# Kernel optimization log

Hardware: AMD Instinct MI355X
Metric: run time of the kernel (lower is better)

The kernel has to match this reference:

```python
import jax, jax.numpy as jnp
import numpy as np

N_NODES = 10000
N_EDGES = 640000
D = 128


def _sage_conv(x, src, dst, W_l, b, W_r):
    # PyG SAGEConv (mean aggr): out = lin_l(mean_{j in N(i)} x_j) + lin_r(x_i)
    msgs = x[src]                                        # [E, D_in] gather
    agg = jax.ops.segment_sum(msgs, dst, num_segments=N_NODES)  # [N, D_in]
    deg = jax.ops.segment_sum(jnp.ones((src.shape[0],), x.dtype), dst,
                              num_segments=N_NODES)
    agg = agg / jnp.maximum(deg, 1.0)[:, None]           # mean; isolated nodes -> 0
    return agg @ W_l + b + x @ W_r


def setup_inputs() -> dict:
    key = jax.random.key(0)
    ks = jax.random.split(key, 8)
    s = 1.0 / np.sqrt(D)
    return {
        "x": jax.random.normal(ks[0], (N_NODES, D), dtype=jnp.float32),
        "edge_index": jax.random.randint(ks[1], (2, N_EDGES), 0, N_NODES, dtype=jnp.int64),
        "W_l0": jax.random.normal(ks[2], (D, D), dtype=jnp.float32) * s,
        "b0": jnp.zeros((D,), dtype=jnp.float32),
        "W_r0": jax.random.normal(ks[3], (D, D), dtype=jnp.float32) * s,
        "W_l1": jax.random.normal(ks[4], (D, D), dtype=jnp.float32) * s,
        "b1": jnp.zeros((D,), dtype=jnp.float32),
        "W_r1": jax.random.normal(ks[5], (D, D), dtype=jnp.float32) * s,
    }


def reference(x, edge_index, W_l0, b0, W_r0, W_l1, b1, W_r1):
    # Dropout(p=0.3) is identity in eval mode (reference runs inference math).
    src, dst = edge_index[0], edge_index[1]
    h = jax.nn.elu(_sage_conv(x, src, dst, W_l0, b0, W_r0))
    h = jax.nn.elu(_sage_conv(h, src, dst, W_l1, b1, W_r1))
    return h
```

## Files before the change

### kernel.cpp

```cpp
#include <hip/hip_runtime.h>

#define N_NODES 10000
#define N_EDGES 640000
#define D 128
#define MAXDEG 128
#define NBUCK 157
#define BCAP 6144
#define EPT 5
#define ZROW 10000

typedef unsigned int uint;
typedef unsigned short u16;
typedef short bf16x8 __attribute__((ext_vector_type(8)));
typedef float f32x4 __attribute__((ext_vector_type(4)));

__device__ __forceinline__ u16 f2bf(float f) {
    uint u = __float_as_uint(f);
    return (u16)((u + 0x7fffu + ((u >> 16) & 1u)) >> 16);
}
__device__ __forceinline__ float bflo(uint v) { return __uint_as_float(v << 16); }
__device__ __forceinline__ float bfhi(uint v) { return __uint_as_float(v & 0xffff0000u); }

__device__ __forceinline__ int edge_at(const void* ei, int is32, int idx) {
    if (is32) return ((const int*)ei)[idx];
    return (int)((const long long*)ei)[idx];
}

__global__ __launch_bounds__(256)
void binp1_kernel(const void* __restrict__ ei, int* __restrict__ gcount,
                  uint* __restrict__ gbucket) {
    __shared__ int hist[NBUCK];
    __shared__ int base[NBUCK];
    __shared__ int s_is32;
    const int t = threadIdx.x;
    if (t < NBUCK) hist[t] = 0;
    if (t == 0) s_is32 = 0;
    __syncthreads();
    const int e0 = blockIdx.x * (256 * EPT);
    if (((const int*)ei)[2 * (e0 + t) + 1] != 0) s_is32 = 1;
    __syncthreads();
    const int is32 = s_is32;
    uint pk[EPT];
    int  rk[EPT];
#pragma unroll
    for (int i = 0; i < EPT; ++i) {
        int e  = e0 + i * 256 + t;
        int s  = edge_at(ei, is32, e);
        int dn = edge_at(ei, is32, N_EDGES + e);
        pk[i] = ((uint)dn << 16) | (uint)s;
        rk[i] = atomicAdd(&hist[dn >> 6], 1);
    }
    __syncthreads();
    if (t < NBUCK) base[t] = atomicAdd(&gcount[t], hist[t]);
    __syncthreads();
#pragma unroll
    for (int i = 0; i < EPT; ++i) {
        int bkt = (int)(pk[i] >> 22);
        int pos = base[bkt] + rk[i];
        if (pos < BCAP) gbucket[(size_t)bkt * BCAP + pos] = pk[i];
    }
}

__global__ __launch_bounds__(256)
void prep_kernel(const int* __restrict__ gcount, const uint* __restrict__ gbucket,
                 u16* __restrict__ adj, int* __restrict__ deg_g,
                 const float* __restrict__ x, uint* __restrict__ xb2,
                 const float* __restrict__ Wl0, const float* __restrict__ Wr0,
                 const float* __restrict__ Wl1, const float* __restrict__ Wr1,
                 u16* __restrict__ WT0, u16* __restrict__ WT1) {
    const int b = blockIdx.x;
    const int t = threadIdx.x;
    __shared__ __align__(16) u16 tile[64][MAXDEG];
    __shared__ int cur[64];
    if (b < NBUCK) {
        uint* tw = (uint*)&tile[0][0];
#pragma unroll
        for (int q = 0; q < 16; ++q) tw[t + q * 256] = ((uint)ZROW << 16) | ZROW;
        if (t < 64) cur[t] = 0;
        __syncthreads();
        const int total = min(gcount[b], BCAP);
        for (int e = t; e < total; e += 256) {
            uint pk = gbucket[(size_t)b * BCAP + e];
            int ln = (int)((pk >> 16) & 63u);
            int r = atomicAdd(&cur[ln], 1);
            if (r < MAXDEG) tile[ln][r] = (u16)(pk & 0xffffu);
        }
        __syncthreads();
        const int node0 = b * 64;
        if (t < 64 && node0 + t < N_NODES) deg_g[node0 + t] = cur[t];
        const uint4* ts = (const uint4*)&tile[0][0];
#pragma unroll
        for (int q = 0; q < 4; ++q) {
            int i = t + q * 256;
            int node = node0 + (i >> 4);
            if (node < N_NODES) ((uint4*)(adj + (size_t)node * MAXDEG))[i & 15] = ts[i];
        }
    } else if (b < NBUCK + 625) {
        int idx = (b - NBUCK) * 256 + t;
        const float4* p = (const float4*)x + (size_t)idx * 2;
        float4 a = p[0], bb = p[1];
        uint4 r;
        r.x = (uint)f2bf(a.x) | ((uint)f2bf(a.y) << 16);
        r.y = (uint)f2bf(a.z) | ((uint)f2bf(a.w) << 16);
        r.z = (uint)f2bf(bb.x) | ((uint)f2bf(bb.y) << 16);
        r.w = (uint)f2bf(bb.z) | ((uint)f2bf(bb.w) << 16);
        ((uint4*)xb2)[idx] = r;
    } else if (b < NBUCK + 625 + 256) {
        int b2 = b - (NBUCK + 625);
        int layer = b2 >> 7, d = b2 & 127, k = t;
        const float* Wl = layer ? Wl1 : Wl0;
        const float* Wr = layer ? Wr1 : Wr0;
        u16* WT = layer ? WT1 : WT0;
        float v = (k < 128) ? Wl[k * D + d] : Wr[(k - 128) * D + d];
        WT[(size_t)d * 256 + k] = f2bf(v);
    } else {
        if (t < 16) ((uint4*)(xb2 + (size_t)ZROW * 64))[t] = make_uint4(0, 0, 0, 0);
    }
}

__global__ __launch_bounds__(256)
void fused_layer_kernel(const uint* __restrict__ src2, const u16* __restrict__ adj,
                        const int* __restrict__ deg_g, const u16* __restrict__ WT,
                        const float* __restrict__ bias,
                        float* __restrict__ outf ,
                        u16* __restrict__ outb ) {
    __shared__ __align__(16) u16 A_lds[4][256];
    const int t = threadIdx.x;
    const int w = t >> 6, l = t & 63;
    const int nb = blockIdx.x * 4;
    const int node = nb + w;

    const int g = l >> 4, c = l & 15;
    const int half = g >> 1, sh = (g & 1) << 4;
    const int dg = deg_g[node];
    const int cnt = min(dg, MAXDEG);
    const uint4* __restrict__ rowq = (const uint4*)(adj + (size_t)node * MAXDEG);
    float acc[8];
#pragma unroll
    for (int i = 0; i < 8; ++i) acc[i] = 0.f;
    const int nch = (cnt + 15) >> 4;
#pragma unroll 2
    for (int ch = 0; ch < nch; ++ch) {
        uint4 wa = rowq[2 * ch];
        uint4 wb = rowq[2 * ch + 1];
        uint a0 = half ? wa.y : wa.x;
        uint a1 = half ? wa.w : wa.z;
        uint b0 = half ? wb.y : wb.x;
        uint b1 = half ? wb.w : wb.z;
        uint id0 = (a0 >> sh) & 0xffffu;
        uint id1 = (a1 >> sh) & 0xffffu;
        uint id2 = (b0 >> sh) & 0xffffu;
        uint id3 = (b1 >> sh) & 0xffffu;
        uint4 v0 = ((const uint4*)(src2 + (size_t)id0 * 64))[c];
        uint4 v1 = ((const uint4*)(src2 + (size_t)id1 * 64))[c];
        uint4 v2 = ((const uint4*)(src2 + (size_t)id2 * 64))[c];
        uint4 v3 = ((const uint4*)(src2 + (size_t)id3 * 64))[c];
        acc[0] += bflo(v0.x) + bflo(v1.x) + bflo(v2.x) + bflo(v3.x);
        acc[1] += bfhi(v0.x) + bfhi(v1.x) + bfhi(v2.x) + bfhi(v3.x);
        acc[2] += bflo(v0.y) + bflo(v1.y) + bflo(v2.y) + bflo(v3.y);
        acc[3] += bfhi(v0.y) + bfhi(v1.y) + bfhi(v2.y) + bfhi(v3.y);
        acc[4] += bflo(v0.z) + bflo(v1.z) + bflo(v2.z) + bflo(v3.z);
        acc[5] += bfhi(v0.z) + bfhi(v1.z) + bfhi(v2.z) + bfhi(v3.z);
        acc[6] += bflo(v0.w) + bflo(v1.w) + bflo(v2.w) + bflo(v3.w);
        acc[7] += bfhi(v0.w) + bfhi(v1.w) + bfhi(v2.w) + bfhi(v3.w);
    }
#pragma unroll
    for (int i = 0; i < 8; ++i) {
        float r = acc[i];
        r += __shfl_xor(r, 16, 64);
        r += __shfl_xor(r, 32, 64);
        acc[i] = r;
    }
    char* arow = (char*)&A_lds[w][0];
    const int swz = w << 4;
    if (g == 0) {
        float inv = 1.0f / fmaxf((float)dg, 1.0f);
        uint4 o;
        o.x = (uint)f2bf(acc[0] * inv) | ((uint)f2bf(acc[1] * inv) << 16);
        o.y = (uint)f2bf(acc[2] * inv) | ((uint)f2bf(acc[3] * inv) << 16);
        o.z = (uint)f2bf(acc[4] * inv) | ((uint)f2bf(acc[5] * inv) << 16);
        o.w = (uint)f2bf(acc[6] * inv) | ((uint)f2bf(acc[7] * inv) << 16);
        *(uint4*)(arow + ((c * 16) ^ swz)) = o;
    }
    if (l < 16) {
        uint4 vx = ((const uint4*)(src2 + (size_t)node * 64))[l];
        *(uint4*)(arow + ((256 + l * 16) ^ swz)) = vx;
    }
    __syncthreads();

    const int lr = l & 15, q = l >> 4;
    f32x4 acc0 = {0.f, 0.f, 0.f, 0.f}, acc1 = {0.f, 0.f, 0.f, 0.f};
    const u16* wt0 = WT + (size_t)(w * 32 + lr) * 256;
    const u16* wt1 = WT + (size_t)(w * 32 + 16 + lr) * 256;
    const char* abase = (const char*)&A_lds[lr & 3][0];
    const int aswz = (lr & 3) << 4;
#pragma unroll
    for (int kk = 0; kk < 8; ++kk) {
        bf16x8 af = {0, 0, 0, 0, 0, 0, 0, 0};
        if (lr < 4) af = *(const bf16x8*)(abase + ((kk * 64 + q * 16) ^ aswz));
        bf16x8 bf0 = *(const bf16x8*)(wt0 + kk * 32 + q * 8);
        bf16x8 bf1 = *(const bf16x8*)(wt1 + kk * 32 + q * 8);
        acc0 = __builtin_amdgcn_mfma_f32_16x16x32_bf16(af, bf0, acc0, 0, 0, 0);
        acc1 = __builtin_amdgcn_mfma_f32_16x16x32_bf16(af, bf1, acc1, 0, 0, 0);
    }
    if (q == 0) {
        const int col0 = w * 32 + lr, col1 = col0 + 16;
        const float b0v = bias[col0], b1v = bias[col1];
#pragma unroll
        for (int j = 0; j < 4; ++j) {
            const int nd = nb + j;
            float v0 = acc0[j] + b0v; v0 = v0 > 0.f ? v0 : expm1f(v0);
            float v1 = acc1[j] + b1v; v1 = v1 > 0.f ? v1 : expm1f(v1);
            if (outf) {
                outf[(size_t)nd * D + col0] = v0;
                outf[(size_t)nd * D + col1] = v1;
            }
            if (outb) {
                outb[(size_t)nd * D + col0] = f2bf(v0);
                outb[(size_t)nd * D + col1] = f2bf(v1);
            }
        }
    }
    if (outb && blockIdx.x == 0 && t < 16)
        ((uint4*)(outb + (size_t)ZROW * D))[t] = make_uint4(0, 0, 0, 0);
}

extern "C" void kernel_launch(void* const* d_in, const int* in_sizes, int n_in,
                              void* d_out, int out_size, void* d_ws, size_t ws_size,
                              hipStream_t stream) {
    const float* x   = (const float*)d_in[0];
    const void*  ei  = d_in[1];
    const float* Wl0 = (const float*)d_in[2];
    const float* b0  = (const float*)d_in[3];
    const float* Wr0 = (const float*)d_in[4];
    const float* Wl1 = (const float*)d_in[5];
    const float* b1  = (const float*)d_in[6];
    const float* Wr1 = (const float*)d_in[7];
    float* out = (float*)d_out;

    char* ws = (char*)d_ws;
    int*  gcount  = (int*)(ws + 1024);
    int*  deg     = (int*)(ws + 4096);
    u16*  adj     = (u16*)(ws + 65536);
    uint* gbucket = (uint*)(ws + 3145728);
    uint* xb2     = (uint*)(ws + 7340032);
    uint* yb2     = (uint*)(ws + 10485760);
    u16*  WT0     = (u16*)(ws + 13631488);
    u16*  WT1     = (u16*)(ws + 13697024);

    hipMemsetAsync(ws, 0, 4096, stream);

    binp1_kernel<<<500, 256, 0, stream>>>(ei, gcount, gbucket);
    prep_kernel<<<NBUCK + 625 + 256 + 1, 256, 0, stream>>>(
        gcount, gbucket, adj, deg, x, xb2, Wl0, Wr0, Wl1, Wr1, WT0, WT1);

    fused_layer_kernel<<<2500, 256, 0, stream>>>(xb2, adj, deg, WT0, b0,
                                                 (float*)0, (u16*)yb2);
    fused_layer_kernel<<<2500, 256, 0, stream>>>(yb2, adj, deg, WT1, b1,
                                                 out, (u16*)0);
}
```

Before: 95.71 us.

## Merge all stages into one cooperative persistent kernel with grid syncs

Replaces the four kernel launches with a single cooperative mega-kernel that bins edges, converts x and the weights, sorts buckets, and runs both SAGE layers, separated by grid.sync barriers. It is meant to remove launch gaps and tail effects between stages. The fused layer now handles 16 nodes per tile, so the MFMA uses all 16 rows instead of 4 with zero padding. A fallback path using separate gather and GEMM kernels is kept. The grid-wide barriers and the limited number of resident persistent blocks (512) could reduce gather parallelism compared with 2500 blocks.

```diff
diff --git a/kernel.cpp b/kernel.cpp
--- a/kernel.cpp
+++ b/kernel.cpp
@@ -1,4 +1,7 @@
 #include <hip/hip_runtime.h>
+#include <hip/hip_cooperative_groups.h>
+
+namespace cg = cooperative_groups;
 
 #define N_NODES 10000
 #define N_EDGES 640000
@@ -6,8 +9,9 @@
 #define MAXDEG 128
 #define NBUCK 157
 #define BCAP 6144
-#define EPT 5
 #define ZROW 10000
+#define NCHUNK 500
+#define CH_E 1280
 
 typedef unsigned int uint;
 typedef unsigned short u16;
@@ -26,24 +30,18 @@
     return (int)((const long long*)ei)[idx];
 }
 
-__global__ __launch_bounds__(256)
-void binp1_kernel(const void* __restrict__ ei, int* __restrict__ gcount,
-                  uint* __restrict__ gbucket) {
-    __shared__ int hist[NBUCK];
-    __shared__ int base[NBUCK];
-    __shared__ int s_is32;
+
+__device__ __forceinline__ void bin_chunk(const void* __restrict__ ei, int is32,
+                                          int chunk, int* hist, int* base,
+                                          int* __restrict__ gcount,
+                                          uint* __restrict__ gbucket) {
     const int t = threadIdx.x;
     if (t < NBUCK) hist[t] = 0;
-    if (t == 0) s_is32 = 0;
-    __syncthreads();
-    const int e0 = blockIdx.x * (256 * EPT);
-    if (((const int*)ei)[2 * (e0 + t) + 1] != 0) s_is32 = 1;
-    __syncthreads();
-    const int is32 = s_is32;
-    uint pk[EPT];
-    int  rk[EPT];
-#pragma unroll
-    for (int i = 0; i < EPT; ++i) {
+    __syncthreads();
+    const int e0 = chunk * CH_E;
+    uint pk[5]; int rk[5];
+#pragma unroll
+    for (int i = 0; i < 5; ++i) {
         int e  = e0 + i * 256 + t;
         int s  = edge_at(ei, is32, e);
         int dn = edge_at(ei, is32, N_EDGES + e);
@@ -54,85 +52,49 @@
     if (t < NBUCK) base[t] = atomicAdd(&gcount[t], hist[t]);
     __syncthreads();
 #pragma unroll
-    for (int i = 0; i < EPT; ++i) {
+    for (int i = 0; i < 5; ++i) {
         int bkt = (int)(pk[i] >> 22);
         int pos = base[bkt] + rk[i];
         if (pos < BCAP) gbucket[(size_t)bkt * BCAP + pos] = pk[i];
     }
 }
 
-__global__ __launch_bounds__(256)
-void prep_kernel(const int* __restrict__ gcount, const uint* __restrict__ gbucket,
-                 u16* __restrict__ adj, int* __restrict__ deg_g,
-                 const float* __restrict__ x, uint* __restrict__ xb2,
-                 const float* __restrict__ Wl0, const float* __restrict__ Wr0,
-                 const float* __restrict__ Wl1, const float* __restrict__ Wr1,
-                 u16* __restrict__ WT0, u16* __restrict__ WT1) {
-    const int b = blockIdx.x;
-    const int t = threadIdx.x;
-    __shared__ __align__(16) u16 tile[64][MAXDEG];
-    __shared__ int cur[64];
-    if (b < NBUCK) {
-        uint* tw = (uint*)&tile[0][0];
-#pragma unroll
-        for (int q = 0; q < 16; ++q) tw[t + q * 256] = ((uint)ZROW << 16) | ZROW;
-        if (t < 64) cur[t] = 0;
-        __syncthreads();
-        const int total = min(gcount[b], BCAP);
-        for (int e = t; e < total; e += 256) {
-            uint pk = gbucket[(size_t)b * BCAP + e];
-            int ln = (int)((pk >> 16) & 63u);
-            int r = atomicAdd(&cur[ln], 1);
-            if (r < MAXDEG) tile[ln][r] = (u16)(pk & 0xffffu);
-        }
-        __syncthreads();
-        const int node0 = b * 64;
-        if (t < 64 && node0 + t < N_NODES) deg_g[node0 + t] = cur[t];
-        const uint4* ts = (const uint4*)&tile[0][0];
-#pragma unroll
-        for (int q = 0; q < 4; ++q) {
-            int i = t + q * 256;
-            int node = node0 + (i >> 4);
-            if (node < N_NODES) ((uint4*)(adj + (size_t)node * MAXDEG))[i & 15] = ts[i];
-        }
-    } else if (b < NBUCK + 625) {
-        int idx = (b - NBUCK) * 256 + t;
-        const float4* p = (const float4*)x + (size_t)idx * 2;
-        float4 a = p[0], bb = p[1];
-        uint4 r;
-        r.x = (uint)f2bf(a.x) | ((uint)f2bf(a.y) << 16);
-        r.y = (uint)f2bf(a.z) | ((uint)f2bf(a.w) << 16);
-        r.z = (uint)f2bf(bb.x) | ((uint)f2bf(bb.y) << 16);
-        r.w = (uint)f2bf(bb.z) | ((uint)f2bf(bb.w) << 16);
-        ((uint4*)xb2)[idx] = r;
-    } else if (b < NBUCK + 625 + 256) {
-        int b2 = b - (NBUCK + 625);
-        int layer = b2 >> 7, d = b2 & 127, k = t;
-        const float* Wl = layer ? Wl1 : Wl0;
-        const float* Wr = layer ? Wr1 : Wr0;
-        u16* WT = layer ? WT1 : WT0;
-        float v = (k < 128) ? Wl[k * D + d] : Wr[(k - 128) * D + d];
-        WT[(size_t)d * 256 + k] = f2bf(v);
-    } else {
-        if (t < 16) ((uint4*)(xb2 + (size_t)ZROW * 64))[t] = make_uint4(0, 0, 0, 0);
-    }
-}
-
-__global__ __launch_bounds__(256)
-void fused_layer_kernel(const uint* __restrict__ src2, const u16* __restrict__ adj,
-                        const int* __restrict__ deg_g, const u16* __restrict__ WT,
-                        const float* __restrict__ bias,
-                        float* __restrict__ outf ,
-                        u16* __restrict__ outb ) {
-    __shared__ __align__(16) u16 A_lds[4][256];
-    const int t = threadIdx.x;
-    const int w = t >> 6, l = t & 63;
-    const int nb = blockIdx.x * 4;
-    const int node = nb + w;
-
-    const int g = l >> 4, c = l & 15;
-    const int half = g >> 1, sh = (g & 1) << 4;
-    const int dg = deg_g[node];
+__device__ __forceinline__ void sort_bucket(char* smem, int b,
+                                            const int* __restrict__ gcount,
+                                            const uint* __restrict__ gbucket,
+                                            u16* __restrict__ adj,
+                                            int* __restrict__ deg_g) {
+    const int t = threadIdx.x;
+    u16 (*tile)[MAXDEG] = (u16 (*)[MAXDEG])smem;
+    int* cur = (int*)(smem + 16384);
+    uint* tw = (uint*)smem;
+#pragma unroll
+    for (int q = 0; q < 16; ++q) tw[t + q * 256] = ((uint)ZROW << 16) | ZROW;
+    if (t < 64) cur[t] = 0;
+    __syncthreads();
+    const int total = min(gcount[b], BCAP);
+    for (int e = t; e < total; e += 256) {
+        uint pk = gbucket[(size_t)b * BCAP + e];
+        int ln = (int)((pk >> 16) & 63u);
+        int r = atomicAdd(&cur[ln], 1);
+        if (r < MAXDEG) tile[ln][r] = (u16)(pk & 0xffffu);
+    }
+    __syncthreads();
+    const int node0 = b * 64;
+    if (t < 64 && node0 + t < N_NODES) deg_g[node0 + t] = cur[t];
+    const uint4* ts = (const uint4*)smem;
+#pragma unroll
+    for (int q = 0; q < 4; ++q) {
+        int i = t + q * 256;
+        int node = node0 + (i >> 4);
+        if (node < N_NODES) ((uint4*)(adj + (size_t)node * MAXDEG))[i & 15] = ts[i];
+    }
+}
+
+__device__ __forceinline__ void gather_node(const uint* __restrict__ src2,
+                                            const u16* __restrict__ adj,
+                                            int node, int dg, int g, int c,
+                                            int half, int sh, uint4* o) {
     const int cnt = min(dg, MAXDEG);
     const uint4* __restrict__ rowq = (const uint4*)(adj + (size_t)node * MAXDEG);
     float acc[8];
@@ -171,58 +133,232 @@
         r += __shfl_xor(r, 32, 64);
         acc[i] = r;
     }
-    char* arow = (char*)&A_lds[w][0];
-    const int swz = w << 4;
-    if (g == 0) {
-        float inv = 1.0f / fmaxf((float)dg, 1.0f);
-        uint4 o;
-        o.x = (uint)f2bf(acc[0] * inv) | ((uint)f2bf(acc[1] * inv) << 16);
-        o.y = (uint)f2bf(acc[2] * inv) | ((uint)f2bf(acc[3] * inv) << 16);
-        o.z = (uint)f2bf(acc[4] * inv) | ((uint)f2bf(acc[5] * inv) << 16);
-        o.w = (uint)f2bf(acc[6] * inv) | ((uint)f2bf(acc[7] * inv) << 16);
-        *(uint4*)(arow + ((c * 16) ^ swz)) = o;
-    }
-    if (l < 16) {
-        uint4 vx = ((const uint4*)(src2 + (size_t)node * 64))[l];
-        *(uint4*)(arow + ((256 + l * 16) ^ swz)) = vx;
-    }
-    __syncthreads();
-
+    float inv = 1.0f / fmaxf((float)dg, 1.0f);
+    o->x = (uint)f2bf(acc[0] * inv) | ((uint)f2bf(acc[1] * inv) << 16);
+    o->y = (uint)f2bf(acc[2] * inv) | ((uint)f2bf(acc[3] * inv) << 16);
+    o->z = (uint)f2bf(acc[4] * inv) | ((uint)f2bf(acc[5] * inv) << 16);
+    o->w = (uint)f2bf(acc[6] * inv) | ((uint)f2bf(acc[7] * inv) << 16);
+}
+
+__device__ __forceinline__ void gemm_tile(const u16* A, int nb,
+                                          const u16* __restrict__ WT,
+                                          const float* __restrict__ bias,
+                                          float* outf, u16* outb) {
+    const int t = threadIdx.x;
+    const int w = t >> 6, l = t & 63;
     const int lr = l & 15, q = l >> 4;
     f32x4 acc0 = {0.f, 0.f, 0.f, 0.f}, acc1 = {0.f, 0.f, 0.f, 0.f};
     const u16* wt0 = WT + (size_t)(w * 32 + lr) * 256;
     const u16* wt1 = WT + (size_t)(w * 32 + 16 + lr) * 256;
-    const char* abase = (const char*)&A_lds[lr & 3][0];
-    const int aswz = (lr & 3) << 4;
+    const char* abase = (const char*)(A + lr * 256);
+    const int aswz = (lr & 7) << 4;
 #pragma unroll
     for (int kk = 0; kk < 8; ++kk) {
-        bf16x8 af = {0, 0, 0, 0, 0, 0, 0, 0};
-        if (lr < 4) af = *(const bf16x8*)(abase + ((kk * 64 + q * 16) ^ aswz));
+        bf16x8 af  = *(const bf16x8*)(abase + ((kk * 64 + q * 16) ^ aswz));
         bf16x8 bf0 = *(const bf16x8*)(wt0 + kk * 32 + q * 8);
         bf16x8 bf1 = *(const bf16x8*)(wt1 + kk * 32 + q * 8);
         acc0 = __builtin_amdgcn_mfma_f32_16x16x32_bf16(af, bf0, acc0, 0, 0, 0);
         acc1 = __builtin_amdgcn_mfma_f32_16x16x32_bf16(af, bf1, acc1, 0, 0, 0);
     }
-    if (q == 0) {
-        const int col0 = w * 32 + lr, col1 = col0 + 16;
-        const float b0v = bias[col0], b1v = bias[col1];
-#pragma unroll
-        for (int j = 0; j < 4; ++j) {
-            const int nd = nb + j;
-            float v0 = acc0[j] + b0v; v0 = v0 > 0.f ? v0 : expm1f(v0);
-            float v1 = acc1[j] + b1v; v1 = v1 > 0.f ? v1 : expm1f(v1);
-            if (outf) {
-                outf[(size_t)nd * D + col0] = v0;
-                outf[(size_t)nd * D + col1] = v1;
-            }
-            if (outb) {
-                outb[(size_t)nd * D + col0] = f2bf(v0);
-                outb[(size_t)nd * D + col1] = f2bf(v1);
+    const int col0 = w * 32 + lr, col1 = col0 + 16;
+    const float b0v = bias[col0], b1v = bias[col1];
+#pragma unroll
+    for (int j = 0; j < 4; ++j) {
+        const int nd = nb + q * 4 + j;
+        float v0 = acc0[j] + b0v; v0 = v0 > 0.f ? v0 : expm1f(v0);
+        float v1 = acc1[j] + b1v; v1 = v1 > 0.f ? v1 : expm1f(v1);
+        if (outf) {
+            outf[(size_t)nd * D + col0] = v0;
+            outf[(size_t)nd * D + col1] = v1;
+        }
+        if (outb) {
+            outb[(size_t)nd * D + col0] = f2bf(v0);
+            outb[(size_t)nd * D + col1] = f2bf(v1);
+        }
+    }
+}
+
+__global__ __launch_bounds__(256)
+void binp1_kernel(const void* __restrict__ ei, int* __restrict__ gcount,
+                  uint* __restrict__ gbucket) {
+    __shared__ int hist[NBUCK];
+    __shared__ int base[NBUCK];
+    __shared__ int s_is32;
+    const int t = threadIdx.x;
+    if (t == 0) s_is32 = 0;
+    __syncthreads();
+    if (((const int*)ei)[2 * t + 1] != 0) s_is32 = 1;
+    __syncthreads();
+    bin_chunk(ei, s_is32, blockIdx.x, hist, base, gcount, gbucket);
+}
+
+__global__ __launch_bounds__(256)
+void prep_kernel(const int* __restrict__ gcount, const uint* __restrict__ gbucket,
+                 u16* __restrict__ adj, int* __restrict__ deg_g,
+                 const float* __restrict__ x, uint* __restrict__ xb2,
+                 const float* __restrict__ Wl0, const float* __restrict__ Wr0,
+                 const float* __restrict__ Wl1, const float* __restrict__ Wr1,
+                 u16* __restrict__ WT0, u16* __restrict__ WT1) {
+    __shared__ __align__(16) char smem[16640];
+    const int b = blockIdx.x;
+    const int t = threadIdx.x;
+    if (b < NBUCK) {
+        sort_bucket(smem, b, gcount, gbucket, adj, deg_g);
+    } else if (b < NBUCK + 625) {
+        int idx = (b - NBUCK) * 256 + t;
+        const float4* p = (const float4*)x + (size_t)idx * 2;
+        float4 a = p[0], bb = p[1];
+        uint4 r;
+        r.x = (uint)f2bf(a.x) | ((uint)f2bf(a.y) << 16);
+        r.y = (uint)f2bf(a.z) | ((uint)f2bf(a.w) << 16);
+        r.z = (uint)f2bf(bb.x) | ((uint)f2bf(bb.y) << 16);
+        r.w = (uint)f2bf(bb.z) | ((uint)f2bf(bb.w) << 16);
+        ((uint4*)xb2)[idx] = r;
+    } else if (b < NBUCK + 625 + 256) {
+        int b2 = b - (NBUCK + 625);
+        int layer = b2 >> 7, d = b2 & 127, k = t;
+        const float* Wl = layer ? Wl1 : Wl0;
+        const float* Wr = layer ? Wr1 : Wr0;
+        u16* WT = layer ? WT1 : WT0;
+        float v = (k < 128) ? Wl[k * D + d] : Wr[(k - 128) * D + d];
+        WT[(size_t)d * 256 + k] = f2bf(v);
+    } else {
+        if (t < 16) ((uint4*)(xb2 + (size_t)ZROW * 64))[t] = make_uint4(0, 0, 0, 0);
+    }
+}
+
+__global__ __launch_bounds__(256)
+void gather_kernel(const uint* __restrict__ xb2, const u16* __restrict__ adj,
+                   const int* __restrict__ deg_g, uint* __restrict__ aggb2) {
+    const int node = blockIdx.x * 4 + (threadIdx.x >> 6);
+    const int l = threadIdx.x & 63;
+    const int g = l >> 4, c = l & 15;
+    const int half = g >> 1, sh = (g & 1) << 4;
+    uint4 o;
+    gather_node(xb2, adj, node, deg_g[node], g, c, half, sh, &o);
+    if (g == 0) ((uint4*)(aggb2 + (size_t)node * 64))[c] = o;
+}
+
+__global__ __launch_bounds__(256)
+void mfma_gemm_kernel(const uint* __restrict__ aggb2, const uint* __restrict__ xb2,
+                      const u16* __restrict__ WT, const float* __restrict__ bias,
+                      float* __restrict__ outf, u16* __restrict__ outb) {
+    __shared__ __align__(16) u16 A_lds[16 * 256];
+    const int t = threadIdx.x;
+    const int nb = blockIdx.x * 16;
+    {
+        const int row = t >> 4, c = t & 15;
+        const int node = nb + row;
+        uint4 va = ((const uint4*)(aggb2 + (size_t)node * 64))[c];
+        uint4 vx = ((const uint4*)(xb2  + (size_t)node * 64))[c];
+        char* base = (char*)A_lds + row * 512;
+        const int swz = (row & 7) << 4;
+        *(uint4*)(base + ((c * 16) ^ swz))       = va;
+        *(uint4*)(base + ((256 + c * 16) ^ swz)) = vx;
+    }
+    __syncthreads();
+    gemm_tile(A_lds, nb, WT, bias, outf, outb);
+    if (outb && blockIdx.x == 0 && t < 16)
+        ((uint4*)(outb + (size_t)ZROW * D))[t] = make_uint4(0, 0, 0, 0);
+}
+
+__device__ __forceinline__ void fused_layer(char* smem, const uint* __restrict__ src2,
+                                            const u16* __restrict__ adj,
+                                            const int* __restrict__ deg_g,
+                                            const u16* __restrict__ WT,
+                                            const float* __restrict__ bias,
+                                            float* outf, u16* outb) {
+    const int t = threadIdx.x;
+    const int w = t >> 6, l = t & 63;
+    const int g = l >> 4, c = l & 15;
+    const int half = g >> 1, sh = (g & 1) << 4;
+    u16* A = (u16*)smem;
+
+    for (int tile = blockIdx.x; tile < 625; tile += gridDim.x) {
+        __syncthreads();
+        const int nb = tile * 16;
+        for (int i = 0; i < 4; ++i) {
+            const int li = w * 4 + i;
+            const int node = nb + li;
+            uint4 o;
+            gather_node(src2, adj, node, deg_g[node], g, c, half, sh, &o);
+            char* arow = (char*)(A + li * 256);
+            const int swz = (li & 7) << 4;
+            if (g == 0) *(uint4*)(arow + ((c * 16) ^ swz)) = o;
+            if (g == 1) {
+                uint4 vx = ((const uint4*)(src2 + (size_t)node * 64))[c];
+                *(uint4*)(arow + ((256 + c * 16) ^ swz)) = vx;
             }
         }
-    }
-    if (outb && blockIdx.x == 0 && t < 16)
-        ((uint4*)(outb + (size_t)ZROW * D))[t] = make_uint4(0, 0, 0, 0);
+        __syncthreads();
+        gemm_tile(A, nb, WT, bias, outf, outb);
+    }
+}
+
+__global__ __launch_bounds__(256, 2)
+void mega_kernel(const void* __restrict__ ei, int* __restrict__ gcount,
+                 uint* __restrict__ gbucket, u16* __restrict__ adj,
+                 int* __restrict__ deg_g, const float* __restrict__ x,
+                 uint* __restrict__ xb2, uint* __restrict__ yb2,
+                 const float* __restrict__ Wl0, const float* __restrict__ Wr0,
+                 const float* __restrict__ Wl1, const float* __restrict__ Wr1,
+                 u16* __restrict__ WT0, u16* __restrict__ WT1,
+                 const float* __restrict__ b0, const float* __restrict__ b1,
+                 float* __restrict__ out) {
+    __shared__ __align__(16) char smem[16640];
+    cg::grid_group grid = cg::this_grid();
+    const int t = threadIdx.x;
+    const int b = blockIdx.x;
+    const int nbk = gridDim.x;
+
+    {
+        int* hist = (int*)smem;
+        int* base = hist + NBUCK;
+        int* s32p = base + NBUCK;
+        if (t == 0) *s32p = 0;
+        __syncthreads();
+        if (((const int*)ei)[2 * t + 1] != 0) *s32p = 1;
+        __syncthreads();
+        const int is32 = *s32p;
+        for (int chunk = b; chunk < NCHUNK; chunk += nbk)
+            bin_chunk(ei, is32, chunk, hist, base, gcount, gbucket);
+    }
+    for (int idx = b * 256 + t; idx < N_NODES * D / 8; idx += nbk * 256) {
+        const float4* p = (const float4*)x + (size_t)idx * 2;
+        float4 a = p[0], bb = p[1];
+        uint4 r;
+        r.x = (uint)f2bf(a.x) | ((uint)f2bf(a.y) << 16);
+        r.y = (uint)f2bf(a.z) | ((uint)f2bf(a.w) << 16);
+        r.z = (uint)f2bf(bb.x) | ((uint)f2bf(bb.y) << 16);
+        r.w = (uint)f2bf(bb.z) | ((uint)f2bf(bb.w) << 16);
+        ((uint4*)xb2)[idx] = r;
+    }
+    for (int idx = b * 256 + t; idx < 2 * D * 256; idx += nbk * 256) {
+        int layer = idx >> 15;
+        int rem = idx & 32767;
+        int d = rem >> 8, k = rem & 255;
+        const float* Wl = layer ? Wl1 : Wl0;
+        const float* Wr = layer ? Wr1 : Wr0;
+        u16* WT = layer ? WT1 : WT0;
+        float v = (k < 128) ? Wl[k * D + d] : Wr[(k - 128) * D + d];
+        WT[(size_t)d * 256 + k] = f2bf(v);
+    }
+    if (b == 0 && t < 16) {
+        ((uint4*)(xb2 + (size_t)ZROW * 64))[t] = make_uint4(0, 0, 0, 0);
+        ((uint4*)(yb2 + (size_t)ZROW * 64))[t] = make_uint4(0, 0, 0, 0);
+    }
+    grid.sync();
+
+    for (int bk = b; bk < NBUCK; bk += nbk) {
+        __syncthreads();
+        sort_bucket(smem, bk, gcount, gbucket, adj, deg_g);
+    }
+    grid.sync();
+
+    fused_layer(smem, xb2, adj, deg_g, WT0, b0, (float*)0, (u16*)yb2);
+    grid.sync();
+
+    fused_layer(smem, yb2, adj, deg_g, WT1, b1, out, (u16*)0);
 }
 
 extern "C" void kernel_launch(void* const* d_in, const int* in_sizes, int n_in,
@@ -245,17 +381,37 @@
     uint* gbucket = (uint*)(ws + 3145728);
     uint* xb2     = (uint*)(ws + 7340032);
     uint* yb2     = (uint*)(ws + 10485760);
-    u16*  WT0     = (u16*)(ws + 13631488);
-    u16*  WT1     = (u16*)(ws + 13697024);
-
-    hipMemsetAsync(ws, 0, 4096, stream);
-
-    binp1_kernel<<<500, 256, 0, stream>>>(ei, gcount, gbucket);
-    prep_kernel<<<NBUCK + 625 + 256 + 1, 256, 0, stream>>>(
-        gcount, gbucket, adj, deg, x, xb2, Wl0, Wr0, Wl1, Wr1, WT0, WT1);
-
-    fused_layer_kernel<<<2500, 256, 0, stream>>>(xb2, adj, deg, WT0, b0,
-                                                 (float*)0, (u16*)yb2);
-    fused_layer_kernel<<<2500, 256, 0, stream>>>(yb2, adj, deg, WT1, b1,
-                                                 out, (u16*)0);
-}
+    uint* aggb2   = (uint*)(ws + 13631488);
+    u16*  WT0     = (u16*)(ws + 16777216);
+    u16*  WT1     = (u16*)(ws + 16842752);
+
+    (void)hipMemsetAsync(ws, 0, 4096, stream);
+
+    int maxB = 0;
+    if (hipOccupancyMaxActiveBlocksPerMultiprocessor(
+            &maxB, (const void*)mega_kernel, 256, 0) != hipSuccess)
+        maxB = 0;
+
+    hipError_t lerr = hipErrorUnknown;
+    if (maxB >= 1) {
+        int gridsz = (maxB >= 2) ? 512 : 256;
+        void* kargs[] = { (void*)&ei, (void*)&gcount, (void*)&gbucket, (void*)&adj,
+                          (void*)&deg, (void*)&x, (void*)&xb2, (void*)&yb2,
+                          (void*)&Wl0, (void*)&Wr0, (void*)&Wl1, (void*)&Wr1,
+                          (void*)&WT0, (void*)&WT1, (void*)&b0, (void*)&b1,
+                          (void*)&out };
+        lerr = hipLaunchCooperativeKernel((const void*)mega_kernel, dim3(gridsz),
+                                          dim3(256), kargs, 0, stream);
+    }
+    if (lerr != hipSuccess) {
+        binp1_kernel<<<NCHUNK, 256, 0, stream>>>(ei, gcount, gbucket);
+        prep_kernel<<<NBUCK + 625 + 256 + 1, 256, 0, stream>>>(
+            gcount, gbucket, adj, deg, x, xb2, Wl0, Wr0, Wl1, Wr1, WT0, WT1);
+        gather_kernel<<<2500, 256, 0, stream>>>(xb2, adj, deg, aggb2);
+        mfma_gemm_kernel<<<625, 256, 0, stream>>>(aggb2, xb2, WT0, b0,
+                                                  (float*)0, (u16*)yb2);
+        gather_kernel<<<2500, 256, 0, stream>>>(yb2, adj, deg, aggb2);
+        mfma_gemm_kernel<<<625, 256, 0, stream>>>(aggb2, yb2, WT1, b1,
+                                                  out, (u16*)0);
+    }
+}
```

Result: slower. 208.9 us (+118.2%).

## Process 16 nodes per block so MFMA tiles use all rows

Applied to the files above, without the earlier changes.

The fused layer kernel now uses 1024-thread blocks that aggregate 16 nodes, one per wave, into LDS. Eight waves then each run one 16x16x32 MFMA chain over all 16 rows, where before only 4 of 16 A rows were real nodes and the rest were zero padding. This removes wasted MFMA work and halves the weight loads per node. The zero-row write for the second layer's input moves into the prep kernel. The cost is a block-wide barrier over 16 waves with half of them idle during the matmul, and lower scheduling flexibility.

```diff
diff --git a/kernel.cpp b/kernel.cpp
--- a/kernel.cpp
+++ b/kernel.cpp
@@ -65,6 +65,7 @@
 void prep_kernel(const int* __restrict__ gcount, const uint* __restrict__ gbucket,
                  u16* __restrict__ adj, int* __restrict__ deg_g,
                  const float* __restrict__ x, uint* __restrict__ xb2,
+                 uint* __restrict__ yb2,
                  const float* __restrict__ Wl0, const float* __restrict__ Wr0,
                  const float* __restrict__ Wl1, const float* __restrict__ Wr1,
                  u16* __restrict__ WT0, u16* __restrict__ WT1) {
@@ -114,115 +115,107 @@
         float v = (k < 128) ? Wl[k * D + d] : Wr[(k - 128) * D + d];
         WT[(size_t)d * 256 + k] = f2bf(v);
     } else {
-        if (t < 16) ((uint4*)(xb2 + (size_t)ZROW * 64))[t] = make_uint4(0, 0, 0, 0);
-    }
-}
-
-__global__ __launch_bounds__(256)
-void fused_layer_kernel(const uint* __restrict__ src2, const u16* __restrict__ adj,
-                        const int* __restrict__ deg_g, const u16* __restrict__ WT,
-                        const float* __restrict__ bias,
-                        float* __restrict__ outf ,
-                        u16* __restrict__ outb ) {
-    __shared__ __align__(16) u16 A_lds[4][256];
+        if (t < 16) {
+            ((uint4*)(xb2 + (size_t)ZROW * 64))[t] = make_uint4(0, 0, 0, 0);
+            ((uint4*)(yb2 + (size_t)ZROW * 64))[t] = make_uint4(0, 0, 0, 0);
+        }
+    }
+}
+
+__global__ __launch_bounds__(1024, 8)
+void fused_kernel(const uint* __restrict__ src2, const u16* __restrict__ adj,
+                  const int* __restrict__ deg_g, const u16* __restrict__ WT,
+                  const float* __restrict__ bias,
+                  float* __restrict__ outf ,
+                  u16* __restrict__ outb ) {
+    __shared__ __align__(16) u16 A_lds[16 * 256];
     const int t = threadIdx.x;
     const int w = t >> 6, l = t & 63;
-    const int nb = blockIdx.x * 4;
+    const int nb = blockIdx.x * 16;
     const int node = nb + w;
 
-    const int g = l >> 4, c = l & 15;
-    const int half = g >> 1, sh = (g & 1) << 4;
-    const int dg = deg_g[node];
-    const int cnt = min(dg, MAXDEG);
-    const uint4* __restrict__ rowq = (const uint4*)(adj + (size_t)node * MAXDEG);
-    float acc[8];
-#pragma unroll
-    for (int i = 0; i < 8; ++i) acc[i] = 0.f;
-    const int nch = (cnt + 15) >> 4;
+    {
+        const int g = l >> 4, c = l & 15;
+        const int half = g >> 1, sh = (g & 1) << 4;
+        const int dg = deg_g[node];
+        const int cnt = min(dg, MAXDEG);
+        const uint4* __restrict__ rowq = (const uint4*)(adj + (size_t)node * MAXDEG);
+        float acc[8];
+#pragma unroll
+        for (int i = 0; i < 8; ++i) acc[i] = 0.f;
+        const int nch = (cnt + 15) >> 4;
 #pragma unroll 2
-    for (int ch = 0; ch < nch; ++ch) {
-        uint4 wa = rowq[2 * ch];
-        uint4 wb = rowq[2 * ch + 1];
-        uint a0 = half ? wa.y : wa.x;
-        uint a1 = half ? wa.w : wa.z;
-        uint b0 = half ? wb.y : wb.x;
-        uint b1 = half ? wb.w : wb.z;
-        uint id0 = (a0 >> sh) & 0xffffu;
-        uint id1 = (a1 >> sh) & 0xffffu;
-        uint id2 = (b0 >> sh) & 0xffffu;
-        uint id3 = (b1 >> sh) & 0xffffu;
-        uint4 v0 = ((const uint4*)(src2 + (size_t)id0 * 64))[c];
-        uint4 v1 = ((const uint4*)(src2 + (size_t)id1 * 64))[c];
-        uint4 v2 = ((const uint4*)(src2 + (size_t)id2 * 64))[c];
-        uint4 v3 = ((const uint4*)(src2 + (size_t)id3 * 64))[c];
-        acc[0] += bflo(v0.x) + bflo(v1.x) + bflo(v2.x) + bflo(v3.x);
-        acc[1] += bfhi(v0.x) + bfhi(v1.x) + bfhi(v2.x) + bfhi(v3.x);
-        acc[2] += bflo(v0.y) + bflo(v1.y) + bflo(v2.y) + bflo(v3.y);
-        acc[3] += bfhi(v0.y) + bfhi(v1.y) + bfhi(v2.y) + bfhi(v3.y);
-        acc[4] += bflo(v0.z) + bflo(v1.z) + bflo(v2.z) + bflo(v3.z);
-        acc[5] += bfhi(v0.z) + bfhi(v1.z) + bfhi(v2.z) + bfhi(v3.z);
-        acc[6] += bflo(v0.w) + bflo(v1.w) + bflo(v2.w) + bflo(v3.w);
-        acc[7] += bfhi(v0.w) + bfhi(v1.w) + bfhi(v2.w) + bfhi(v3.w);
-    }
-#pragma unroll
-    for (int i = 0; i < 8; ++i) {
-        float r = acc[i];
-        r += __shfl_xor(r, 16, 64);
-        r += __shfl_xor(r, 32, 64);
-        acc[i] = r;
-    }
-    char* arow = (char*)&A_lds[w][0];
-    const int swz = w << 4;
-    if (g == 0) {
-        float inv = 1.0f / fmaxf((float)dg, 1.0f);
-        uint4 o;
-        o.x = (uint)f2bf(acc[0] * inv) | ((uint)f2bf(acc[1] * inv) << 16);
-        o.y = (uint)f2bf(acc[2] * inv) | ((uint)f2bf(acc[3] * inv) << 16);
-        o.z = (uint)f2bf(acc[4] * inv) | ((uint)f2bf(acc[5] * inv) << 16);
-        o.w = (uint)f2bf(acc[6] * inv) | ((uint)f2bf(acc[7] * inv) << 16);
-        *(uint4*)(arow + ((c * 16) ^ swz)) = o;
-    }
-    if (l < 16) {
-        uint4 vx = ((const uint4*)(src2 + (size_t)node * 64))[l];
-        *(uint4*)(arow + ((256 + l * 16) ^ swz)) = vx;
-    }
-    __syncthreads();
-
-    const int lr = l & 15, q = l >> 4;
-    f32x4 acc0 = {0.f, 0.f, 0.f, 0.f}, acc1 = {0.f, 0.f, 0.f, 0.f};
-    const u16* wt0 = WT + (size_t)(w * 32 + lr) * 256;
-    const u16* wt1 = WT + (size_t)(w * 32 + 16 + lr) * 256;
-    const char* abase = (const char*)&A_lds[lr & 3][0];
-    const int aswz = (lr & 3) << 4;
-#pragma unroll
-    for (int kk = 0; kk < 8; ++kk) {
-        bf16x8 af = {0, 0, 0, 0, 0, 0, 0, 0};
-        if (lr < 4) af = *(const bf16x8*)(abase + ((kk * 64 + q * 16) ^ aswz));
-        bf16x8 bf0 = *(const bf16x8*)(wt0 + kk * 32 + q * 8);
-        bf16x8 bf1 = *(const bf16x8*)(wt1 + kk * 32 + q * 8);
-        acc0 = __builtin_amdgcn_mfma_f32_16x16x32_bf16(af, bf0, acc0, 0, 0, 0);
-        acc1 = __builtin_amdgcn_mfma_f32_16x16x32_bf16(af, bf1, acc1, 0, 0, 0);
-    }
-    if (q == 0) {
-        const int col0 = w * 32 + lr, col1 = col0 + 16;
-        const float b0v = bias[col0], b1v = bias[col1];
+        for (int ch = 0; ch < nch; ++ch) {
+            uint4 wa = rowq[2 * ch];
+            uint4 wb = rowq[2 * ch + 1];
+            uint a0 = half ? wa.y : wa.x;
+            uint a1 = half ? wa.w : wa.z;
+            uint b0 = half ? wb.y : wb.x;
+            uint b1 = half ? wb.w : wb.z;
+            uint id0 = (a0 >> sh) & 0xffffu;
+            uint id1 = (a1 >> sh) & 0xffffu;
+            uint id2 = (b0 >> sh) & 0xffffu;
+            uint id3 = (b1 >> sh) & 0xffffu;
+            uint4 v0 = ((const uint4*)(src2 + (size_t)id0 * 64))[c];
+            uint4 v1 = ((const uint4*)(src2 + (size_t)id1 * 64))[c];
+            uint4 v2 = ((const uint4*)(src2 + (size_t)id2 * 64))[c];
+            uint4 v3 = ((const uint4*)(src2 + (size_t)id3 * 64))[c];
+            acc[0] += bflo(v0.x) + bflo(v1.x) + bflo(v2.x) + bflo(v3.x);
+            acc[1] += bfhi(v0.x) + bfhi(v1.x) + bfhi(v2.x) + bfhi(v3.x);
+            acc[2] += bflo(v0.y) + bflo(v1.y) + bflo(v2.y) + bflo(v3.y);
+            acc[3] += bfhi(v0.y) + bfhi(v1.y) + bfhi(v2.y) + bfhi(v3.y);
+            acc[4] += bflo(v0.z) + bflo(v1.z) + bflo(v2.z) + bflo(v3.z);
+            acc[5] += bfhi(v0.z) + bfhi(v1.z) + bfhi(v2.z) + bfhi(v3.z);
+            acc[6] += bflo(v0.w) + bflo(v1.w) + bflo(v2.w) + bflo(v3.w);
+            acc[7] += bfhi(v0.w) + bfhi(v1.w) + bfhi(v2.w) + bfhi(v3.w);
+        }
+#pragma unroll
+        for (int i = 0; i < 8; ++i) {
+            float r = acc[i];
+            r += __shfl_xor(r, 16, 64);
+            r += __shfl_xor(r, 32, 64);
+            acc[i] = r;
+        }
+        char* arow = (char*)A_lds + w * 512;
+        const int swz = (w & 7) << 4;
+        if (g == 0) {
+            float inv = 1.0f / fmaxf((float)dg, 1.0f);
+            uint4 o;
+            o.x = (uint)f2bf(acc[0] * inv) | ((uint)f2bf(acc[1] * inv) << 16);
+            o.y = (uint)f2bf(acc[2] * inv) | ((uint)f2bf(acc[3] * inv) << 16);
+            o.z = (uint)f2bf(acc[4] * inv) | ((uint)f2bf(acc[5] * inv) << 16);
+            o.w = (uint)f2bf(acc[6] * inv) | ((uint)f2bf(acc[7] * inv) << 16);
+            *(uint4*)(arow + ((c * 16) ^ swz)) = o;
+        } else if (g == 1) {
+            uint4 vx = ((const uint4*)(src2 + (size_t)node * 64))[c];
+            *(uint4*)(arow + ((256 + c * 16) ^ swz)) = vx;
+        }
+    }
+    __syncthreads();
+
+    if (w < 8) {
+        const int lr = l & 15, q = l >> 4;
+        f32x4 acc0 = {0.f, 0.f, 0.f, 0.f};
+        const u16* wt = WT + (size_t)(w * 16 + lr) * 256;
+        const char* abase = (const char*)A_lds + lr * 512;
+        const int aswz = (lr & 7) << 4;
+#pragma unroll
+        for (int kk = 0; kk < 8; ++kk) {
+            bf16x8 af = *(const bf16x8*)(abase + ((kk * 64 + q * 16) ^ aswz));
+            bf16x8 bf = *(const bf16x8*)(wt + kk * 32 + q * 8);
+            acc0 = __builtin_amdgcn_mfma_f32_16x16x32_bf16(af, bf, acc0, 0, 0, 0);
+        }
+        const int col = w * 16 + lr;
+        const float bv = bias[col];
 #pragma unroll
         for (int j = 0; j < 4; ++j) {
-            const int nd = nb + j;
-            float v0 = acc0[j] + b0v; v0 = v0 > 0.f ? v0 : expm1f(v0);
-            float v1 = acc1[j] + b1v; v1 = v1 > 0.f ? v1 : expm1f(v1);
-            if (outf) {
-                outf[(size_t)nd * D + col0] = v0;
-                outf[(size_t)nd * D + col1] = v1;
-            }
-            if (outb) {
-                outb[(size_t)nd * D + col0] = f2bf(v0);
-                outb[(size_t)nd * D + col1] = f2bf(v1);
-            }
-        }
-    }
-    if (outb && blockIdx.x == 0 && t < 16)
-        ((uint4*)(outb + (size_t)ZROW * D))[t] = make_uint4(0, 0, 0, 0);
+            const int nd = nb + q * 4 + j;
+            float v = acc0[j] + bv;
+            v = v > 0.f ? v : expm1f(v);
+            if (outf) outf[(size_t)nd * D + col] = v;
+            if (outb) outb[(size_t)nd * D + col] = f2bf(v);
+        }
+    }
 }
 
 extern "C" void kernel_launch(void* const* d_in, const int* in_sizes, int n_in,
@@ -248,14 +241,14 @@
     u16*  WT0     = (u16*)(ws + 13631488);
     u16*  WT1     = (u16*)(ws + 13697024);
 
-    hipMemsetAsync(ws, 0, 4096, stream);
+    (void)hipMemsetAsync(ws, 0, 4096, stream);
 
     binp1_kernel<<<500, 256, 0, stream>>>(ei, gcount, gbucket);
     prep_kernel<<<NBUCK + 625 + 256 + 1, 256, 0, stream>>>(
-        gcount, gbucket, adj, deg, x, xb2, Wl0, Wr0, Wl1, Wr1, WT0, WT1);
-
-    fused_layer_kernel<<<2500, 256, 0, stream>>>(xb2, adj, deg, WT0, b0,
-                                                 (float*)0, (u16*)yb2);
-    fused_layer_kernel<<<2500, 256, 0, stream>>>(yb2, adj, deg, WT1, b1,
-                                                 out, (u16*)0);
-}
+        gcount, gbucket, adj, deg, x, xb2, yb2, Wl0, Wr0, Wl1, Wr1, WT0, WT1);
+
+    fused_kernel<<<625, 1024, 0, stream>>>(xb2, adj, deg, WT0, b0,
+                                           (float*)0, (u16*)yb2);
+    fused_kernel<<<625, 1024, 0, stream>>>(yb2, adj, deg, WT1, b1,
+                                           out, (u16*)0);
+}
```

Result: faster. 77.12 us, median of 2 (-19.4%).
